# Performance work log

Measured on AMD Instinct MI355X. Metric: run time of the kernel, lower is better.

The kernel has to match this reference:

```python
import jax, jax.numpy as jnp
import numpy as np

C_T = 64
C_OUT = 128
RANK = 8
LN_EPS = 1e-5


def setup_inputs() -> dict:
    key = jax.random.key(0)
    ks = jax.random.split(key, 8)
    B, L = 1, 768
    feat = jax.random.normal(ks[0], (B, L, L, C_T), dtype=jnp.float32)
    Wq = jax.random.normal(ks[1], (C_T, 1), dtype=jnp.float32) / np.sqrt(C_T)
    bq = jnp.zeros((1,), dtype=jnp.float32)
    ln_g = jnp.ones((C_T * 3,), dtype=jnp.float32)
    ln_b = jnp.zeros((C_T * 3,), dtype=jnp.float32)
    WU = jax.random.normal(ks[2], (C_T * 3, RANK * C_OUT), dtype=jnp.float32) / np.sqrt(C_T * 3)
    bU = jnp.zeros((RANK * C_OUT,), dtype=jnp.float32)
    WV = jax.random.normal(ks[3], (C_T * 3, RANK * C_OUT), dtype=jnp.float32) / np.sqrt(C_T * 3)
    bV = jnp.zeros((RANK * C_OUT,), dtype=jnp.float32)
    sigma = jnp.ones((RANK,), dtype=jnp.float32)
    return {"template_feat": feat, "Wq": Wq, "bq": bq, "ln_g": ln_g, "ln_b": ln_b,
            "WU": WU, "bU": bU, "WV": WV, "bV": bV, "sigma": sigma}


def _layer_norm(x, g, b):
    mu = jnp.mean(x, axis=-1, keepdims=True)
    var = jnp.mean(jnp.square(x - mu), axis=-1, keepdims=True)
    return (x - mu) * jax.lax.rsqrt(var + LN_EPS) * g + b


def reference(template_feat, Wq, bq, ln_g, ln_b, WU, bU, WV, bV, sigma):
    B, L, _, C = template_feat.shape
    rank = sigma.shape[0]
    c_out = WU.shape[1] // rank
    # attention logits, shared by both pools: [B, L, L]
    logits = jnp.einsum('bijc,co->bijo', template_feat, Wq)[..., 0] + bq[0]
    # row pool: softmax over j (dim=2)
    w_row = jax.nn.softmax(logits, axis=2)
    row_feat = jnp.einsum('bij,bijc->bic', w_row, template_feat)
    # col pool: softmax over i (dim=1)
    w_col = jax.nn.softmax(logits, axis=1)
    col_feat = jnp.einsum('bij,bijc->bjc', w_col, template_feat)
    # diagonal gather: [B, L, C]
    idx = jnp.arange(L)
    diag_feat = template_feat[:, idx, idx, :]
    left = _layer_norm(jnp.concatenate([diag_feat, row_feat, col_feat], axis=-1), ln_g, ln_b)
    right = _layer_norm(jnp.concatenate([diag_feat, col_feat, row_feat], axis=-1), ln_g, ln_b)
    template_left = (left @ WU + bU).reshape(B, L, rank, c_out)
    template_right = (right @ WV + bV).reshape(B, L, rank, c_out)
    template_left = template_left * sigma[None, None, :, None]
    return (template_left, template_right)
```

## Files before the change

### kernel.cpp

```cpp
#include <hip/hip_runtime.h>
#include <math.h>

#define LL 768
#define CT 64
#define KD 192
#define OC 1024
#define TS 16
#define NST 48
#define PCH 68

__device__ __forceinline__ float sum16(float x) {
    x += __int_as_float(__builtin_amdgcn_update_dpp(0, __float_as_int(x), 0xB1, 0xF, 0xF, true));
    x += __int_as_float(__builtin_amdgcn_update_dpp(0, __float_as_int(x), 0x4E, 0xF, 0xF, true));
    x += __int_as_float(__builtin_amdgcn_update_dpp(0, __float_as_int(x), 0x124, 0xF, 0xF, true));
    x += __int_as_float(__builtin_amdgcn_update_dpp(0, __float_as_int(x), 0x128, 0xF, 0xF, true));
    return x;
}

__global__ __launch_bounds__(256, 6) void k_fused(const float* __restrict__ feat,
                                                  const float* __restrict__ Wq,
                                                  const float* __restrict__ bq,
                                                  float* __restrict__ rp,
                                                  float* __restrict__ cp) {
    __shared__ float4 lbuf[16][8][17];
    __shared__ float  zb[16][9];

    int t = threadIdx.x;
    int u = t >> 4, q = t & 15;
    int bj = blockIdx.x, bi = blockIdx.y;
    int i0 = bi * TS, j0 = bj * TS;

    const float4 wq = *reinterpret_cast<const float4*>(Wq + q * 4);
    const float bqv = bq[0];

    const float* fb = feat + ((size_t)i0 * LL + j0 + u) * CT + q * 4;
    const size_t istr = (size_t)LL * CT;
    float4 creg = make_float4(0.f, 0.f, 0.f, 0.f);
    float zc = 0.f;

    float4 fnext = *reinterpret_cast<const float4*>(fb);

    #pragma unroll 2
    for (int half = 0; half < 2; ++half) {
        #pragma unroll
        for (int ii = 0; ii < 8; ++ii) {
            const int idx = half * 8 + ii;
            const float4 f = fnext;
            if (idx < 15)
                fnext = *reinterpret_cast<const float4*>(fb + (size_t)(idx + 1) * istr);

            float s = f.x * wq.x + f.y * wq.y + f.z * wq.z + f.w * wq.w;
            s = sum16(s);
            float e = __expf(s + bqv);

            float4 p;
            p.x = e * f.x; p.y = e * f.y; p.z = e * f.z; p.w = e * f.w;

            creg.x += p.x; creg.y += p.y; creg.z += p.z; creg.w += p.w;
            zc += e;

            lbuf[u][ii][q] = p;
            if (q == 0) zb[u][ii] = e;
        }
        __syncthreads();

        if (t < 128) {
            int ii = t >> 4, c4 = t & 15;
            float4 a = make_float4(0.f, 0.f, 0.f, 0.f);
            #pragma unroll
            for (int uu = 0; uu < 16; ++uu) {
                const float4 v = lbuf[uu][ii][c4];
                a.x += v.x; a.y += v.y; a.z += v.z; a.w += v.w;
            }
            *reinterpret_cast<float4*>(rp + ((size_t)(i0 + half * 8 + ii) * NST + bj) * PCH
                                       + c4 * 4) = a;
        }
        if (t < 8) {
            float zz = 0.f;
            #pragma unroll
            for (int uu = 0; uu < 16; ++uu) zz += zb[uu][t];
            rp[((size_t)(i0 + half * 8 + t) * NST + bj) * PCH + 64] = zz;
        }
        __syncthreads();
    }

    size_t cpo = ((size_t)(j0 + u) * NST + bi) * PCH;
    *reinterpret_cast<float4*>(cp + cpo + q * 4) = creg;
    if (q == 0) cp[cpo + 64] = zc;
}

__global__ __launch_bounds__(256) void k_combine(const float* __restrict__ rp,
                                                 const float* __restrict__ cp,
                                                 float* __restrict__ rcfeat) {
    int t = threadIdx.x;
    int r = t >> 4, q = t & 15;
    int L = blockIdx.x * 16 + r;
    int side = blockIdx.y;
    const float* base = (side ? cp : rp) + (size_t)L * NST * PCH;

    float4 acc = make_float4(0.f, 0.f, 0.f, 0.f);
    float z = 0.f;
    #pragma unroll 4
    for (int s = 0; s < NST; ++s) {
        const float4 v = *reinterpret_cast<const float4*>(base + s * PCH + q * 4);
        acc.x += v.x; acc.y += v.y; acc.z += v.z; acc.w += v.w;
        z += base[s * PCH + 64];
    }
    float inv = 1.0f / z;
    acc.x *= inv; acc.y *= inv; acc.z *= inv; acc.w *= inv;
    *reinterpret_cast<float4*>(rcfeat + (size_t)side * LL * CT
                               + (size_t)L * CT + q * 4) = acc;
}

__global__ __launch_bounds__(256) void k_final(const float* __restrict__ feat,
                                               const float* __restrict__ rcfeat,
                                               const float* __restrict__ ln_g,
                                               const float* __restrict__ ln_b,
                                               const float* __restrict__ WU,
                                               const float* __restrict__ bU,
                                               const float* __restrict__ WV,
                                               const float* __restrict__ bV,
                                               const float* __restrict__ sigma,
                                               float* __restrict__ out) {
    __shared__ float xbuf[8][KD];
    int t = threadIdx.x;
    int wid = t >> 6, l = t & 63;
    int r0 = blockIdx.x * 8;
    int right = blockIdx.y;
    const float* rfeat = rcfeat;
    const float* cfeat = rcfeat + LL * CT;

    for (int r = wid; r < 8; r += 4) {
        int i = r0 + r;
        float d  = feat[((size_t)i * LL + i) * CT + l];
        float rv = rfeat[(size_t)i * CT + l];
        float cv = cfeat[(size_t)i * CT + l];
        float sum = d + rv + cv;
        #pragma unroll
        for (int o = 32; o; o >>= 1) sum += __shfl_xor(sum, o);
        float mu = sum * (1.0f / 192.0f);
        float d0 = d - mu, d1 = rv - mu, d2 = cv - mu;
        float sq = d0 * d0 + d1 * d1 + d2 * d2;
        #pragma unroll
        for (int o = 32; o; o >>= 1) sq += __shfl_xor(sq, o);
        float rstd = rsqrtf(sq * (1.0f / 192.0f) + 1e-5f);
        float h0 = d0 * rstd, h1 = d1 * rstd, h2 = d2 * rstd;
        float a1 = right ? h2 : h1;
        float a2 = right ? h1 : h2;
        xbuf[r][l]       = h0 * ln_g[l]       + ln_b[l];
        xbuf[r][64 + l]  = a1 * ln_g[64 + l]  + ln_b[64 + l];
        xbuf[r][128 + l] = a2 * ln_g[128 + l] + ln_b[128 + l];
    }
    __syncthreads();

    const float* W    = right ? WV : WU;
    const float* bias = right ? bV : bU;
    int o = blockIdx.z * 512 + t * 2;
    float2 acc[8];
    #pragma unroll
    for (int r = 0; r < 8; ++r) acc[r] = make_float2(0.f, 0.f);

    for (int k = 0; k < KD; k += 4) {
        float4 xr[8];
        #pragma unroll
        for (int r = 0; r < 8; ++r)
            xr[r] = *reinterpret_cast<const float4*>(&xbuf[r][k]);
        #pragma unroll
        for (int kk = 0; kk < 4; ++kk) {
            const float2 wv = *reinterpret_cast<const float2*>(W + (size_t)(k + kk) * OC + o);
            #pragma unroll
            for (int r = 0; r < 8; ++r) {
                float xv = (&xr[r].x)[kk];
                acc[r].x = fmaf(xv, wv.x, acc[r].x);
                acc[r].y = fmaf(xv, wv.y, acc[r].y);
            }
        }
    }

    const float2 bb = *reinterpret_cast<const float2*>(bias + o);
    float sg = right ? 1.0f : sigma[o >> 7];
    float* obase = out + (right ? (size_t)LL * OC : 0);
    #pragma unroll
    for (int r = 0; r < 8; ++r) {
        float2 v;
        v.x = (acc[r].x + bb.x) * sg;
        v.y = (acc[r].y + bb.y) * sg;
        *reinterpret_cast<float2*>(obase + (size_t)(r0 + r) * OC + o) = v;
    }
}

extern "C" void kernel_launch(void* const* d_in, const int* in_sizes, int n_in,
                              void* d_out, int out_size, void* d_ws, size_t ws_size,
                              hipStream_t stream) {
    const float* feat  = (const float*)d_in[0];
    const float* Wq    = (const float*)d_in[1];
    const float* bq    = (const float*)d_in[2];
    const float* ln_g  = (const float*)d_in[3];
    const float* ln_b  = (const float*)d_in[4];
    const float* WU    = (const float*)d_in[5];
    const float* bU    = (const float*)d_in[6];
    const float* WV    = (const float*)d_in[7];
    const float* bV    = (const float*)d_in[8];
    const float* sigma = (const float*)d_in[9];
    float* out = (float*)d_out;

    float* ws     = (float*)d_ws;
    float* rp     = ws;
    float* cp     = rp + (size_t)LL * NST * PCH;
    float* rcfeat = cp + (size_t)LL * NST * PCH;

    hipLaunchKernelGGL(k_fused, dim3(NST, NST), dim3(256), 0, stream,
                       feat, Wq, bq, rp, cp);
    hipLaunchKernelGGL(k_combine, dim3(LL / 16, 2), dim3(256), 0, stream,
                       rp, cp, rcfeat);
    hipLaunchKernelGGL(k_final, dim3(LL / 8, 2, 2), dim3(256), 0, stream,
                       feat, rcfeat, ln_g, ln_b, WU, bU, WV, bV, sigma, out);
}
```

Before: 61.70 us.

## Restructure fused pooling kernel to reduce rows via wave shuffles

The fused logits/softmax-pool kernel now has each wave own 4 rows of the 16x16 tile, with lanes split into 4 column groups. Row partial sums are reduced with cross-lane shuffles inside the wave instead of through shared memory. Column partials are accumulated in registers and combined once through a small shared buffer after a single barrier. This removes two barriers and the larger LDS staging per tile. The per-thread loads are issued as four independent loads per row rather than a rolling prefetch chain, and the occupancy hint of 6 blocks per CU is dropped.

Measured after the change: 61.28 us. Within noise of the previous version (-0.7%).

```diff
diff --git a/kernel.cpp b/kernel.cpp
--- a/kernel.cpp
+++ b/kernel.cpp
@@ -17,76 +17,99 @@
     return x;
 }
 
-__global__ __launch_bounds__(256, 6) void k_fused(const float* __restrict__ feat,
-                                                  const float* __restrict__ Wq,
-                                                  const float* __restrict__ bq,
-                                                  float* __restrict__ rp,
-                                                  float* __restrict__ cp) {
-    __shared__ float4 lbuf[16][8][17];
-    __shared__ float  zb[16][9];
+__global__ __launch_bounds__(256) void k_fused(const float* __restrict__ feat,
+                                               const float* __restrict__ Wq,
+                                               const float* __restrict__ bq,
+                                               float* __restrict__ rp,
+                                               float* __restrict__ cp) {
+    __shared__ float cpart[4][16][68];
 
     int t = threadIdx.x;
-    int u = t >> 4, q = t & 15;
+    int w = t >> 6, ln = t & 63;
+    int g = ln >> 4, q = ln & 15;
     int bj = blockIdx.x, bi = blockIdx.y;
     int i0 = bi * TS, j0 = bj * TS;
 
     const float4 wq = *reinterpret_cast<const float4*>(Wq + q * 4);
     const float bqv = bq[0];
 
-    const float* fb = feat + ((size_t)i0 * LL + j0 + u) * CT + q * 4;
-    const size_t istr = (size_t)LL * CT;
-    float4 creg = make_float4(0.f, 0.f, 0.f, 0.f);
-    float zc = 0.f;
-
-    float4 fnext = *reinterpret_cast<const float4*>(fb);
-
-    #pragma unroll 2
-    for (int half = 0; half < 2; ++half) {
-        #pragma unroll
-        for (int ii = 0; ii < 8; ++ii) {
-            const int idx = half * 8 + ii;
-            const float4 f = fnext;
-            if (idx < 15)
-                fnext = *reinterpret_cast<const float4*>(fb + (size_t)(idx + 1) * istr);
-
-            float s = f.x * wq.x + f.y * wq.y + f.z * wq.z + f.w * wq.w;
-            s = sum16(s);
-            float e = __expf(s + bqv);
-
-            float4 p;
-            p.x = e * f.x; p.y = e * f.y; p.z = e * f.z; p.w = e * f.w;
-
-            creg.x += p.x; creg.y += p.y; creg.z += p.z; creg.w += p.w;
-            zc += e;
-
-            lbuf[u][ii][q] = p;
-            if (q == 0) zb[u][ii] = e;
+    float4 c0 = make_float4(0,0,0,0), c1 = make_float4(0,0,0,0);
+    float4 c2 = make_float4(0,0,0,0), c3 = make_float4(0,0,0,0);
+    float zc0 = 0.f, zc1 = 0.f, zc2 = 0.f, zc3 = 0.f;
+
+    #define STEP(F, CR, ZC)                                              \
+        {                                                                \
+            float s = F.x * wq.x + F.y * wq.y + F.z * wq.z + F.w * wq.w; \
+            s = sum16(s);                                                \
+            float e = __expf(s + bqv);                                   \
+            float4 p;                                                    \
+            p.x = e * F.x; p.y = e * F.y; p.z = e * F.z; p.w = e * F.w;  \
+            racc.x += p.x; racc.y += p.y; racc.z += p.z; racc.w += p.w;  \
+            zr += e;                                                     \
+            CR.x += p.x; CR.y += p.y; CR.z += p.z; CR.w += p.w;          \
+            ZC += e;                                                     \
         }
-        __syncthreads();
-
-        if (t < 128) {
-            int ii = t >> 4, c4 = t & 15;
-            float4 a = make_float4(0.f, 0.f, 0.f, 0.f);
-            #pragma unroll
-            for (int uu = 0; uu < 16; ++uu) {
-                const float4 v = lbuf[uu][ii][c4];
-                a.x += v.x; a.y += v.y; a.z += v.z; a.w += v.w;
-            }
-            *reinterpret_cast<float4*>(rp + ((size_t)(i0 + half * 8 + ii) * NST + bj) * PCH
-                                       + c4 * 4) = a;
+
+    #pragma unroll
+    for (int r = 0; r < 4; ++r) {
+        const int row = i0 + w * 4 + r;
+        const float* fb = feat + ((size_t)row * LL + j0 + g) * CT + q * 4;
+
+        const float4 f0 = *reinterpret_cast<const float4*>(fb + 0 * 4 * CT);
+        const float4 f1 = *reinterpret_cast<const float4*>(fb + 1 * 4 * CT);
+        const float4 f2 = *reinterpret_cast<const float4*>(fb + 2 * 4 * CT);
+        const float4 f3 = *reinterpret_cast<const float4*>(fb + 3 * 4 * CT);
+
+        float4 racc = make_float4(0,0,0,0);
+        float zr = 0.f;
+        STEP(f0, c0, zc0)
+        STEP(f1, c1, zc1)
+        STEP(f2, c2, zc2)
+        STEP(f3, c3, zc3)
+
+        racc.x += __shfl_xor(racc.x, 16); racc.x += __shfl_xor(racc.x, 32);
+        racc.y += __shfl_xor(racc.y, 16); racc.y += __shfl_xor(racc.y, 32);
+        racc.z += __shfl_xor(racc.z, 16); racc.z += __shfl_xor(racc.z, 32);
+        racc.w += __shfl_xor(racc.w, 16); racc.w += __shfl_xor(racc.w, 32);
+        zr     += __shfl_xor(zr, 16);     zr     += __shfl_xor(zr, 32);
+
+        if (g == 0) {
+            size_t ro = ((size_t)row * NST + bj) * PCH;
+            *reinterpret_cast<float4*>(rp + ro + q * 4) = racc;
+            if (q == 0) rp[ro + 64] = zr;
         }
-        if (t < 8) {
-            float zz = 0.f;
-            #pragma unroll
-            for (int uu = 0; uu < 16; ++uu) zz += zb[uu][t];
-            rp[((size_t)(i0 + half * 8 + t) * NST + bj) * PCH + 64] = zz;
-        }
-        __syncthreads();
-    }
-
-    size_t cpo = ((size_t)(j0 + u) * NST + bi) * PCH;
-    *reinterpret_cast<float4*>(cp + cpo + q * 4) = creg;
-    if (q == 0) cp[cpo + 64] = zc;
+    }
+    #undef STEP
+
+    *reinterpret_cast<float4*>(&cpart[w][0 * 4 + g][q * 4]) = c0;
+    *reinterpret_cast<float4*>(&cpart[w][1 * 4 + g][q * 4]) = c1;
+    *reinterpret_cast<float4*>(&cpart[w][2 * 4 + g][q * 4]) = c2;
+    *reinterpret_cast<float4*>(&cpart[w][3 * 4 + g][q * 4]) = c3;
+    if (q == 0) {
+        cpart[w][0 * 4 + g][64] = zc0;
+        cpart[w][1 * 4 + g][64] = zc1;
+        cpart[w][2 * 4 + g][64] = zc2;
+        cpart[w][3 * 4 + g][64] = zc3;
+    }
+    __syncthreads();
+
+    {
+        int jj = t >> 4, c4 = t & 15;
+        const float4 a0 = *reinterpret_cast<const float4*>(&cpart[0][jj][c4 * 4]);
+        const float4 a1 = *reinterpret_cast<const float4*>(&cpart[1][jj][c4 * 4]);
+        const float4 a2 = *reinterpret_cast<const float4*>(&cpart[2][jj][c4 * 4]);
+        const float4 a3 = *reinterpret_cast<const float4*>(&cpart[3][jj][c4 * 4]);
+        float4 a;
+        a.x = (a0.x + a1.x) + (a2.x + a3.x);
+        a.y = (a0.y + a1.y) + (a2.y + a3.y);
+        a.z = (a0.z + a1.z) + (a2.z + a3.z);
+        a.w = (a0.w + a1.w) + (a2.w + a3.w);
+        size_t co = ((size_t)(j0 + jj) * NST + bi) * PCH;
+        *reinterpret_cast<float4*>(cp + co + c4 * 4) = a;
+        if (c4 == 0)
+            cp[co + 64] = cpart[0][jj][64] + cpart[1][jj][64]
+                        + cpart[2][jj][64] + cpart[3][jj][64];
+    }
 }
 
 __global__ __launch_bounds__(256) void k_combine(const float* __restrict__ rp,
```
